# Performance work log

Hardware: AMD Instinct MI355X
Metric: run time of the kernel (lower is better)

The kernel has to match this reference:

```python
import jax, jax.numpy as jnp
import numpy as np

N = 20000
CIN = 32
COUT = 64
K = 4              # kernel_size per axis
KF = K * K * K     # 64 kernel bins
EXTENT = 0.1       # filter_extent; search radius = EXTENT/2
E_PAD = 262144
FOUR_OVER_PI = 4.0 / np.pi
EPS = 1e-12


def _safe_sqrt(x):
    # sqrt with zero (not nan) gradient at 0
    return jnp.sqrt(jnp.maximum(x, EPS))


def ball_to_cube_vp(p):
    """Open3D ball_to_cube_volume_preserving: unit ball -> [-1,1]^3 cube.
    p: [E,3] points in the unit ball."""
    x, y, z = p[:, 0], p[:, 1], p[:, 2]
    sq = x * x + y * y + z * z
    norm = _safe_sqrt(sq)
    rxy2 = x * x + y * y
    # --- sphere -> cylinder (volume preserving) ---
    top = 1.25 * z * z > rxy2
    s_top = _safe_sqrt(3.0 * norm / (norm + jnp.abs(z) + EPS))
    s_side = norm / _safe_sqrt(rxy2)
    cx = jnp.where(top, x * s_top, x * s_side)
    cy = jnp.where(top, y * s_top, y * s_side)
    cz = jnp.where(top, jnp.sign(z) * norm, 1.5 * z)
    zero = sq < EPS
    cx = jnp.where(zero, 0.0, cx)
    cy = jnp.where(zero, 0.0, cy)
    cz = jnp.where(zero, 0.0, cz)
    # --- cylinder -> cube (angle preserving square mapping in xy) ---
    rxy = _safe_sqrt(cx * cx + cy * cy)
    xbig = jnp.abs(cy) <= jnp.abs(cx)
    safe_x = jnp.where(jnp.abs(cx) > EPS, cx, 1.0)
    safe_y = jnp.where(jnp.abs(cy) > EPS, cy, 1.0)
    qx = jnp.sign(cx) * rxy
    qy = jnp.sign(cy) * rxy
    bx = jnp.where(xbig, qx, qy * FOUR_OVER_PI * jnp.arctan(cx / safe_y))
    by = jnp.where(xbig, qx * FOUR_OVER_PI * jnp.arctan(cy / safe_x), qy)
    small = cx * cx + cy * cy < EPS
    bx = jnp.where(small, 0.0, bx)
    by = jnp.where(small, 0.0, by)
    return jnp.stack([bx, by, cz], axis=1)


def setup_inputs() -> dict:
    rng = np.random.default_rng(0)
    pos = rng.random((N, 3)).astype(np.float32)
    radius = EXTENT * 0.5
    # chunked brute-force fixed-radius search (ignore self pairs)
    sq_norms = (pos * pos).sum(-1)
    qs, ns = [], []
    chunk = 2000
    for s in range(0, N, chunk):
        blk = pos[s:s + chunk]
        d2 = sq_norms[s:s + chunk, None] + sq_norms[None, :] - 2.0 * blk @ pos.T
        qi, nj = np.nonzero(d2 < radius * radius)
        qi = qi + s
        keep = qi != nj
        qs.append(qi[keep]); ns.append(nj[keep])
    eq = np.concatenate(qs); en = np.concatenate(ns)
    E = eq.shape[0]
    assert E <= E_PAD, E
    edge_q = np.zeros(E_PAD, np.int64); edge_q[:E] = eq
    edge_n = np.zeros(E_PAD, np.int64); edge_n[:E] = en
    edge_valid = np.zeros(E_PAD, np.float32); edge_valid[:E] = 1.0

    key = jax.random.key(0)
    k1, k2, k3, k4 = jax.random.split(key, 4)
    feats = jax.random.normal(k1, (N, CIN), dtype=jnp.float32)
    Wconv = jax.random.normal(k2, (K, K, K, CIN, COUT), dtype=jnp.float32) * 0.05
    Wd = jax.random.normal(k3, (CIN, COUT), dtype=jnp.float32) * 0.05
    bd = jax.random.normal(k4, (COUT,), dtype=jnp.float32) * 0.05
    return {"feats": feats, "pos": jnp.asarray(pos), "Wconv": Wconv,
            "Wd": Wd, "bd": bd,
            "edge_q": jnp.asarray(edge_q), "edge_n": jnp.asarray(edge_n),
            "edge_valid": jnp.asarray(edge_valid)}


def _cconv(feats, pos, Wconv, edge_q, edge_n, edge_valid):
    # relative positions scaled into the unit ball (search radius = EXTENT/2)
    rel = (pos[edge_n] - pos[edge_q]) * (2.0 / EXTENT)          # [E,3]
    cube = ball_to_cube_vp(rel)                                  # [E,3] in [-1,1]^3
    # align_corners=True grid coords
    u = jnp.clip((cube + 1.0) * 0.5 * (K - 1), 0.0, K - 1.0)     # [E,3] (x,y,z)
    i0 = jnp.clip(jnp.floor(u).astype(jnp.int32), 0, K - 2)
    f = u - i0.astype(u.dtype)                                   # trilinear fracs
    fj = feats[edge_n] * edge_valid[:, None]                     # [E,Cin]
    segq = edge_q.astype(jnp.int32) * KF
    # accumulate neighbor feats into per-query kernel bins (8 trilinear corners)
    Z = jnp.zeros((N * KF, CIN), feats.dtype)
    for dz in (0, 1):
        wz = f[:, 2] if dz else 1.0 - f[:, 2]
        for dy in (0, 1):
            wy = f[:, 1] if dy else 1.0 - f[:, 1]
            for dx in (0, 1):
                wx = f[:, 0] if dx else 1.0 - f[:, 0]
                w = wz * wy * wx
                idx = ((i0[:, 2] + dz) * K + (i0[:, 1] + dy)) * K + (i0[:, 0] + dx)
                Z = Z + jax.ops.segment_sum(fj * w[:, None], segq + idx,
                                            num_segments=N * KF)
    # dense contraction against the flattened filter bank
    return jnp.einsum('nki,kio->no', Z.reshape(N, KF, CIN),
                      Wconv.reshape(KF, CIN, COUT))


def reference(feats, pos, Wconv, Wd, bd, edge_q, edge_n, edge_valid):
    ans_conv = _cconv(feats, pos, Wconv, edge_q, edge_n, edge_valid)
    ans_dense = feats @ Wd + bd
    return ans_conv, ans_dense
```

## Files before the change

kernel.cpp:

```cpp
#include <hip/hip_runtime.h>

#define N_PTS 20000
#define CIN   32
#define COUT  64
#define KK    4
#define KF    64
#define KDIM  2048
#define E_PAD 262144
#define EPS   1e-12f
#define FOUR_OVER_PI 1.27323954473516f
#define QB    8
#define MT16  16

#define NB_Q 1024
#define NB_G 1024
#define NB_W 512
#define NB_F 1250
#define NB_D 313

typedef __attribute__((ext_vector_type(8))) short bf16x8;
typedef __attribute__((ext_vector_type(4))) float f32x4;

__device__ __forceinline__ float sgnf(float v) {
    return v > 0.f ? 1.f : (v < 0.f ? -1.f : 0.f);
}
__device__ __forceinline__ int imin(int a, int b) { return a < b ? a : b; }
__device__ __forceinline__ int imax(int a, int b) { return a > b ? a : b; }

__device__ __forceinline__ unsigned short f2bf(float f) {
    unsigned u = __float_as_uint(f);
    u = u + 0x7fffu + ((u >> 16) & 1u);
    return (unsigned short)(u >> 16);
}

__device__ __forceinline__ unsigned cvtpk(float a, float b) {
    unsigned r;
    asm("v_cvt_pk_bf16_f32 %0, %1, %2" : "=v"(r) : "v"(a), "v"(b));
    return r;
}

__device__ __forceinline__ void edge_geom(
    const float* __restrict__ pos, int n, int q,
    int& cellb, float& ofx, float& ofy, float& ofz)
{
    const float rx = (pos[n * 3 + 0] - pos[q * 3 + 0]) * 20.f;
    const float ry = (pos[n * 3 + 1] - pos[q * 3 + 1]) * 20.f;
    const float rz = (pos[n * 3 + 2] - pos[q * 3 + 2]) * 20.f;
    const float sq   = rx * rx + ry * ry + rz * rz;
    const float nrm  = sqrtf(fmaxf(sq, EPS));
    const float rxy2 = rx * rx + ry * ry;
    const bool  top  = (1.25f * rz * rz > rxy2);
    const float s_top  = sqrtf(fmaxf(3.f * nrm / (nrm + fabsf(rz) + EPS), EPS));
    const float s_side = nrm / sqrtf(fmaxf(rxy2, EPS));
    float cx = top ? rx * s_top : rx * s_side;
    float cy = top ? ry * s_top : ry * s_side;
    float cz = top ? sgnf(rz) * nrm : 1.5f * rz;
    if (sq < EPS) { cx = 0.f; cy = 0.f; cz = 0.f; }
    const float rc2 = cx * cx + cy * cy;
    const float rxy = sqrtf(fmaxf(rc2, EPS));
    const bool  xbig = fabsf(cy) <= fabsf(cx);
    const float safe_x = (fabsf(cx) > EPS) ? cx : 1.f;
    const float safe_y = (fabsf(cy) > EPS) ? cy : 1.f;
    const float qxv = sgnf(cx) * rxy;
    const float qyv = sgnf(cy) * rxy;
    float bx = xbig ? qxv : qyv * FOUR_OVER_PI * atanf(cx / safe_y);
    float by = xbig ? qxv * FOUR_OVER_PI * atanf(cy / safe_x) : qyv;
    if (rc2 < EPS) { bx = 0.f; by = 0.f; }
    const float ux = fminf(fmaxf((bx + 1.f) * 0.5f * 3.f, 0.f), 3.f);
    const float uy = fminf(fmaxf((by + 1.f) * 0.5f * 3.f, 0.f), 3.f);
    const float uz = fminf(fmaxf((cz + 1.f) * 0.5f * 3.f, 0.f), 3.f);
    const int ix = imin(imax((int)floorf(ux), 0), 2);
    const int iy = imin(imax((int)floorf(uy), 0), 2);
    const int iz = imin(imax((int)floorf(uz), 0), 2);
    cellb = (iz * KK + iy) * KK + ix;
    ofx = ux - (float)ix; ofy = uy - (float)iy; ofz = uz - (float)iz;
}

__global__ __launch_bounds__(256) void prologue_kernel(
    const float* __restrict__ feats, const float* __restrict__ pos,
    const float* __restrict__ Wconv, const float* __restrict__ Wd,
    const float* __restrict__ bd,
    const int* __restrict__ eq, const int* __restrict__ en,
    const float* __restrict__ ev, int strideQ, int strideN,
    int* __restrict__ qstart, unsigned short* __restrict__ Wfrag,
    unsigned* __restrict__ fbp, float4* __restrict__ rec,
    float* __restrict__ out)
{
    const int bid = blockIdx.x;
    const int tid = threadIdx.x;
    if (bid < NB_Q) {
        const int e = bid * 256 + tid;
        int k = (ev[e] > 0.f) ? eq[e * strideQ] : N_PTS;
        if (k > N_PTS) k = N_PTS;
        int kp = -1;
        if (e > 0) {
            kp = (ev[e - 1] > 0.f) ? eq[(e - 1) * strideQ] : N_PTS;
            if (kp > N_PTS) kp = N_PTS;
        }
        for (int q = kp + 1; q <= k; ++q) qstart[q] = e;
        if (e == E_PAD - 1)
            for (int q = k + 1; q <= N_PTS; ++q) qstart[q] = E_PAD;
    } else if (bid < NB_Q + NB_G) {
        const int e = (bid - NB_Q) * 256 + tid;
        const int q = eq[e * strideQ];
        const int n = en[e * strideN];
        int ib; float fx, fy, fz;
        edge_geom(pos, n, q, ib, fx, fy, fz);
        float4 r;
        r.x = fx; r.y = fy; r.z = fz;
        r.w = __int_as_float(n | (ib << 16) | (1 << 22));
        rec[e] = r;
    } else if (bid < NB_Q + NB_G + NB_W) {
        const int idx = (bid - NB_Q - NB_G) * 256 + tid;
        const int j    = idx & 7;
        const int lane = (idx >> 3) & 63;
        const int nf   = (idx >> 9) & 3;
        const int ks   = idx >> 11;
        const int k    = ks * 32 + ((lane >> 4) << 3) + j;
        const int col  = nf * 16 + (lane & 15);
        Wfrag[idx] = f2bf(Wconv[k * COUT + col]);
    } else if (bid < NB_Q + NB_G + NB_W + NB_F) {
        const int i = (bid - NB_Q - NB_G - NB_W) * 256 + tid;
        const int n = i >> 4, c = i & 15;
        fbp[i] = cvtpk(feats[n * CIN + c], feats[n * CIN + c + 16]);
    } else {
        const int db   = bid - NB_Q - NB_G - NB_W - NB_F;
        const int wv   = tid >> 6, lane = tid & 63;
        const int r16  = lane & 15, kgrp = lane >> 4;
        const int qb   = (db * 4 + wv) * 16;
        if (qb < N_PTS) {
            const float4 f0 = *(const float4*)(feats + (size_t)(qb + r16) * CIN + kgrp * 8);
            const float4 f1 = *(const float4*)(feats + (size_t)(qb + r16) * CIN + kgrp * 8 + 4);
            bf16x8 a8;
            ((unsigned*)&a8)[0] = cvtpk(f0.x, f0.y);
            ((unsigned*)&a8)[1] = cvtpk(f0.z, f0.w);
            ((unsigned*)&a8)[2] = cvtpk(f1.x, f1.y);
            ((unsigned*)&a8)[3] = cvtpk(f1.z, f1.w);
            #pragma unroll
            for (int nf = 0; nf < 4; ++nf) {
                bf16x8 b8;
                #pragma unroll
                for (int jp = 0; jp < 4; ++jp) {
                    const float w0 = Wd[(kgrp * 8 + jp * 2)     * COUT + nf * 16 + r16];
                    const float w1 = Wd[(kgrp * 8 + jp * 2 + 1) * COUT + nf * 16 + r16];
                    ((unsigned*)&b8)[jp] = cvtpk(w0, w1);
                }
                f32x4 acc = {0.f, 0.f, 0.f, 0.f};
                acc = __builtin_amdgcn_mfma_f32_16x16x32_bf16(a8, b8, acc, 0, 0, 0);
                const float bo = bd[nf * 16 + r16];
                #pragma unroll
                for (int rg = 0; rg < 4; ++rg) {
                    const int q = qb + kgrp * 4 + rg;
                    out[(size_t)N_PTS * COUT + q * COUT + nf * 16 + r16] = acc[rg] + bo;
                }
            }
        }
    }
}

__global__ __launch_bounds__(512, 4) void fused_kernel(
    const unsigned* __restrict__ fbp,
    const float4* __restrict__ rec,
    const unsigned short* __restrict__ Wfrag,
    const int* __restrict__ qstart, float* __restrict__ out)
{
    __shared__ __align__(16) unsigned short Zl[MT16 * KDIM];
    __shared__ __align__(16) char scratch[8192];
    float4 (*ebuf)[2][32]   = (float4 (*)[2][32])scratch;
    float  (*partial)[MT16][COUT] = (float (*)[MT16][COUT])scratch;

    const int t    = threadIdx.x;
    const int w    = t >> 6;
    const int lane = t & 63;
    const int r16  = lane & 15;
    const int kgrp = lane >> 4;
    const int q0   = blockIdx.x * MT16;

    const int dxc = r16 & 3, dyc = r16 >> 2;
    {
        const int lo0 = qstart[q0 + w * 2];
        const int hi0 = qstart[q0 + w * 2 + 1];
        const int hi1 = qstart[q0 + w * 2 + 2];
        const int lo1 = hi0;
        const int nch0 = imax(1, (hi0 - lo0 + 31) >> 5);
        const int nch1 = imax(1, (hi1 - lo1 + 31) >> 5);
        const int NC   = nch0 + nch1;

        {
            const int sfi = lane >> 5, l32 = lane & 31;
            const int isq1 = sfi >= nch0;
            const int c    = isq1 ? sfi - nch0 : sfi;
            const int lo   = isq1 ? lo1 : lo0;
            const int hi   = isq1 ? hi1 : hi0;
            const int e    = lo + c * 32 + l32;
            float4 r;
            if (e < hi) r = rec[e];
            else { r.x = 0.f; r.y = 0.f; r.z = 0.f; r.w = __int_as_float(0); }
            ebuf[w][sfi][l32] = r;
        }

        f32x4 acc[2][4];
        #pragma unroll
        for (int mf = 0; mf < 2; ++mf)
            #pragma unroll
            for (int nf = 0; nf < 4; ++nf)
                acc[mf][nf] = (f32x4){0.f, 0.f, 0.f, 0.f};

        for (int fi = 0; fi < NC; ++fi) {
            if (fi == nch0) {
                const int qs = w * 2;
                #pragma unroll
                for (int mf = 0; mf < 2; ++mf)
                    #pragma unroll
                    for (int nf = 0; nf < 4; ++nf) {
                        uint2 dv;
                        dv.x = cvtpk(acc[mf][nf][0], acc[mf][nf][1]);
                        dv.y = cvtpk(acc[mf][nf][2], acc[mf][nf][3]);
                        const int g      = nf * 16 + r16;
                        const int slot   = g * 64 + qs * 4 + mf * 2 + (kgrp >> 1);
                        const int stored = slot ^ (g & 7);
                        *(uint2*)&Zl[stored * 8 + (kgrp & 1) * 4] = dv;
                        acc[mf][nf] = (f32x4){0.f, 0.f, 0.f, 0.f};
                    }
            }
            const float4* buf = ebuf[w][fi & 1];
            bf16x8 bP[4], af[2];
            #pragma unroll
            for (int jp = 0; jp < 4; ++jp) {
                float p[2][4];
                #pragma unroll
                for (int h = 0; h < 2; ++h) {
                    const int j = jp * 2 + h;
                    const float4 r = buf[kgrp * 8 + j];
                    const int meta = __float_as_int(r.w);
                    const int n    = meta & 0xFFFF;
                    const int ib   = (meta >> 16) & 63;
                    const float valid = (meta & (1 << 22)) ? 1.f : 0.f;
                    const int ix = ib & 3, iy = (ib >> 2) & 3, iz = ib >> 4;
                    const float wx = (dxc == ix) ? (1.f - r.x)
                                   : ((dxc == ix + 1) ? r.x : 0.f);
                    const float wy = (dyc == iy) ? (1.f - r.y)
                                   : ((dyc == iy + 1) ? r.y : 0.f);
                    const float wxy = wx * wy * valid;
                    const float z0 = wxy * (1.f - r.z), z1 = wxy * r.z;
                    p[h][0] = (iz == 0) ? z0 : 0.f;
                    p[h][1] = (iz == 0) ? z1 : ((iz == 1) ? z0 : 0.f);
                    p[h][2] = (iz == 2) ? z0 : ((iz == 1) ? z1 : 0.f);
                    p[h][3] = (iz == 2) ? z1 : 0.f;
                    const unsigned uf = fbp[(size_t)n * 16 + r16];
                    af[0][j] = (short)(uf & 0xFFFFu);
                    af[1][j] = (short)(uf >> 16);
                }
                #pragma unroll
                for (int nf = 0; nf < 4; ++nf)
                    ((unsigned*)&bP[nf])[jp] = cvtpk(p[0][nf], p[1][nf]);
            }
            #pragma unroll
            for (int nf = 0; nf < 4; ++nf) {
                acc[0][nf] = __builtin_amdgcn_mfma_f32_16x16x32_bf16(
                    af[0], bP[nf], acc[0][nf], 0, 0, 0);
                acc[1][nf] = __builtin_amdgcn_mfma_f32_16x16x32_bf16(
                    af[1], bP[nf], acc[1][nf], 0, 0, 0);
            }
            const int nfi = fi + 2;
            if (nfi < NC && lane < 32) {
                const int isq1 = nfi >= nch0;
                const int c    = isq1 ? nfi - nch0 : nfi;
                const int lo   = isq1 ? lo1 : lo0;
                const int hi   = isq1 ? hi1 : hi0;
                const int e    = lo + c * 32 + lane;
                float4 r;
                if (e < hi) r = rec[e];
                else { r.x = 0.f; r.y = 0.f; r.z = 0.f;
                       r.w = __int_as_float(0); }
                ebuf[w][fi & 1][lane] = r;
            }
        }
        {
            const int qs = w * 2 + 1;
            #pragma unroll
            for (int mf = 0; mf < 2; ++mf)
                #pragma unroll
                for (int nf = 0; nf < 4; ++nf) {
                    uint2 dv;
                    dv.x = cvtpk(acc[mf][nf][0], acc[mf][nf][1]);
                    dv.y = cvtpk(acc[mf][nf][2], acc[mf][nf][3]);
                    const int g      = nf * 16 + r16;
                    const int slot   = g * 64 + qs * 4 + mf * 2 + (kgrp >> 1);
                    const int stored = slot ^ (g & 7);
                    *(uint2*)&Zl[stored * 8 + (kgrp & 1) * 4] = dv;
                }
        }
    }
    __syncthreads();

    {
        const int kw  = w >> 2;
        const int nfB = w & 3;
        f32x4 acc0 = {0.f, 0.f, 0.f, 0.f};
        f32x4 acc1 = {0.f, 0.f, 0.f, 0.f};
        #pragma unroll 4
        for (int i = 0; i < 16; ++i) {
            const int ksA = kw * 32 + 2 * i;
            const int ksB = ksA + 1;
            const int stA = (ksA * 64 + r16 * 4 + kgrp) ^ (ksA & 7);
            const int stB = (ksB * 64 + r16 * 4 + kgrp) ^ (ksB & 7);
            const bf16x8 aA = *(const bf16x8*)&Zl[stA * 8];
            const bf16x8 aB = *(const bf16x8*)&Zl[stB * 8];
            const bf16x8 bA =
                *(const bf16x8*)(Wfrag + (((ksA * 4 + nfB) * 64) + lane) * 8);
            const bf16x8 bB =
                *(const bf16x8*)(Wfrag + (((ksB * 4 + nfB) * 64) + lane) * 8);
            acc0 = __builtin_amdgcn_mfma_f32_16x16x32_bf16(aA, bA, acc0, 0, 0, 0);
            acc1 = __builtin_amdgcn_mfma_f32_16x16x32_bf16(aB, bB, acc1, 0, 0, 0);
        }
        const f32x4 accB = acc0 + acc1;
        #pragma unroll
        for (int rg = 0; rg < 4; ++rg)
            partial[kw][kgrp * 4 + rg][nfB * 16 + r16] = accB[rg];
    }
    __syncthreads();

    #pragma unroll
    for (int rep = 0; rep < MT16 * COUT / 512; ++rep) {
        const int idx = rep * 512 + t;
        const int r = idx >> 6, o = idx & 63;
        out[(q0 + r) * COUT + o] = partial[0][r][o] + partial[1][r][o];
    }
}

__global__ __launch_bounds__(256) void conv_dense_kernel(
    const float* __restrict__ feats, const float* __restrict__ pos,
    const float* __restrict__ Wconv, const float* __restrict__ Wd,
    const float* __restrict__ bd,
    const int* __restrict__ en, const float* __restrict__ ev,
    const int* __restrict__ qstart, int strideN,
    float* __restrict__ out)
{
    __shared__ float Z[QB][KF][CIN];
    __shared__ float partial[4][QB][COUT];
    __shared__ int   rec_n[256], rec_b[256];
    __shared__ float rec_fx[256], rec_fy[256], rec_fz[256];
    __shared__ int   qs9[QB + 1];

    const int t = threadIdx.x, wave = t >> 6, lane = t & 63;
    const int q0 = blockIdx.x * QB;
    if (t <= QB) qs9[t] = qstart[q0 + t];
    float* zf = &Z[0][0][0];
    for (int j = t; j < QB * KF * CIN; j += 256) zf[j] = 0.f;
    __syncthreads();
    const int eLo = qs9[0], eHi = qs9[QB];
    const int ci = lane & 31, dbase = lane >> 5;
    for (int cb = eLo; cb < eHi; cb += 256) {
        const int cnt = imin(256, eHi - cb);
        if (t < cnt) {
            const int e = cb + t;
            int q = q0;
            #pragma unroll
            for (int s = 1; s < QB; ++s) if (e >= qs9[s]) q = q0 + s;
            int nn = ((const int*)en)[e];
            int ib; float fx, fy, fz;
            edge_geom(pos, nn, q, ib, fx, fy, fz);
            rec_n[t] = nn; rec_b[t] = ib;
            rec_fx[t] = fx; rec_fy[t] = fy; rec_fz[t] = fz;
        }
        __syncthreads();
        for (int s = 0; s < QB / 4; ++s) {
            const int qs = wave * (QB / 4) + s;
            const int lo = imax(qs9[qs], cb);
            const int hi = imin(qs9[qs + 1], cb + cnt);
            for (int e = lo; e < hi; ++e) {
                const int r = e - cb;
                const int n = rec_n[r], ib = rec_b[r];
                const float fx = rec_fx[r], fy = rec_fy[r], fz = rec_fz[r];
                const float fj = feats[n * CIN + ci];
                const float wxf = dbase ? fx : 1.f - fx;
                #pragma unroll
                for (int dd = 0; dd < 4; ++dd) {
                    const int dy = dd & 1, dz = dd >> 1;
                    const float wv = (dz ? fz : 1.f - fz) * (dy ? fy : 1.f - fy) * wxf;
                    Z[qs][ib + dz * 16 + dy * 4 + dbase][ci] += fj * wv;
                }
            }
        }
        __syncthreads();
    }
    float acc[QB];
    #pragma unroll
    for (int qs = 0; qs < QB; ++qs) acc[qs] = 0.f;
    const int o = lane;
    for (int kk = 0; kk < KF / 4; ++kk) {
        const int kf = wave * (KF / 4) + kk;
        #pragma unroll
        for (int ii = 0; ii < CIN; ii += 4) {
            float4 z4[QB];
            #pragma unroll
            for (int qs = 0; qs < QB; ++qs)
                z4[qs] = *(const float4*)&Z[qs][kf][ii];
            #pragma unroll
            for (int c = 0; c < 4; ++c) {
                const float wv = Wconv[(kf * CIN + ii + c) * COUT + o];
                #pragma unroll
                for (int qs = 0; qs < QB; ++qs)
                    acc[qs] += wv * ((const float*)&z4[qs])[c];
            }
        }
    }
    #pragma unroll
    for (int qs = 0; qs < QB; ++qs) partial[wave][qs][o] = acc[qs];
    __syncthreads();
    for (int s = 0; s < QB / 4; ++s) {
        const int qs = wave * (QB / 4) + s;
        const int q  = q0 + qs;
        out[q * COUT + o] = partial[0][qs][o] + partial[1][qs][o] +
                            partial[2][qs][o] + partial[3][qs][o];
        float dacc = bd[o];
        #pragma unroll
        for (int ii = 0; ii < CIN; ++ii)
            dacc += feats[q * CIN + ii] * Wd[ii * COUT + o];
        out[N_PTS * COUT + q * COUT + o] = dacc;
    }
}

__global__ __launch_bounds__(256) void pack_en_kernel(
    const int* __restrict__ en, int stride, int* __restrict__ en32)
{
    const int e = blockIdx.x * 256 + threadIdx.x;
    if (e < E_PAD) en32[e] = en[e * stride];
}

__global__ __launch_bounds__(256) void build_qstart_kernel(
    const int* __restrict__ eq, const float* __restrict__ ev,
    int stride, int* __restrict__ qstart)
{
    int e = blockIdx.x * 256 + threadIdx.x;
    if (e >= E_PAD) return;
    int k = (ev[e] > 0.f) ? eq[e * stride] : N_PTS;
    if (k > N_PTS) k = N_PTS;
    int kp = -1;
    if (e > 0) {
        kp = (ev[e - 1] > 0.f) ? eq[(e - 1) * stride] : N_PTS;
        if (kp > N_PTS) kp = N_PTS;
    }
    for (int q = kp + 1; q <= k; ++q) qstart[q] = e;
    if (e == E_PAD - 1) {
        for (int q = k + 1; q <= N_PTS; ++q) qstart[q] = E_PAD;
    }
}

extern "C" void kernel_launch(void* const* d_in, const int* in_sizes, int n_in,
                              void* d_out, int out_size, void* d_ws, size_t ws_size,
                              hipStream_t stream)
{
    const float* feats = (const float*)d_in[0];
    const float* pos   = (const float*)d_in[1];
    const float* Wconv = (const float*)d_in[2];
    const float* Wd    = (const float*)d_in[3];
    const float* bd    = (const float*)d_in[4];
    const int*   eq    = (const int*)d_in[5];
    const int*   en    = (const int*)d_in[6];
    const float* ev    = (const float*)d_in[7];
    const int strideQ = in_sizes[5] / E_PAD;
    const int strideN = in_sizes[6] / E_PAD;

    int* qstart = (int*)d_ws;
    const size_t offW  = 81920;
    const size_t offFB = offW + 262144;
    const size_t offR  = offFB + (size_t)N_PTS * CIN * 2;
    const size_t needed = offR + (size_t)E_PAD * 16;

    if (ws_size >= needed) {
        unsigned short* Wfrag = (unsigned short*)((char*)d_ws + offW);
        unsigned*       fbp   = (unsigned*)((char*)d_ws + offFB);
        float4*         rec   = (float4*)((char*)d_ws + offR);
        prologue_kernel<<<NB_Q + NB_G + NB_W + NB_F + NB_D, 256, 0, stream>>>(
            feats, pos, Wconv, Wd, bd, eq, en, ev, strideQ, strideN,
            qstart, Wfrag, fbp, rec, (float*)d_out);
        fused_kernel<<<N_PTS / MT16, 512, 0, stream>>>(
            fbp, rec, Wfrag, qstart, (float*)d_out);
    } else {
        build_qstart_kernel<<<E_PAD / 256, 256, 0, stream>>>(
            eq, ev, strideQ, qstart);
        int* en32 = (int*)((char*)d_ws + offW);
        pack_en_kernel<<<E_PAD / 256, 256, 0, stream>>>(en, strideN, en32);
        conv_dense_kernel<<<N_PTS / QB, 256, 0, stream>>>(
            feats, pos, Wconv, Wd, bd, en32, ev, qstart, 1, (float*)d_out);
    }
}
```

Measured before the change: 36.82 us.

## Shrink fused tile to 8 queries, one query per wave, drop edge prefetch

The fused conv kernel now handles 8 queries per 512-thread block instead of 16, so each wave owns a single query rather than two. This removes the mid-loop accumulator flush and the double-buffered edge-record prefetch. The grid doubles, giving more blocks and finer load balance across varying neighbor counts. In exchange, the dense GEMM stage computes 16-row MFMA tiles with only 8 valid rows, wasting half its work, and edge loads are no longer overlapped with compute. The prologue also skips geometry for invalid edges, which leaves their record slots unwritten.

```diff
diff --git a/kernel.cpp b/kernel.cpp
--- a/kernel.cpp
+++ b/kernel.cpp
@@ -10,7 +10,7 @@
 #define EPS   1e-12f
 #define FOUR_OVER_PI 1.27323954473516f
 #define QB    8
-#define MT16  16
+#define MT8   8
 
 #define NB_Q 1024
 #define NB_G 1024
@@ -102,14 +102,16 @@
             for (int q = k + 1; q <= N_PTS; ++q) qstart[q] = E_PAD;
     } else if (bid < NB_Q + NB_G) {
         const int e = (bid - NB_Q) * 256 + tid;
-        const int q = eq[e * strideQ];
-        const int n = en[e * strideN];
-        int ib; float fx, fy, fz;
-        edge_geom(pos, n, q, ib, fx, fy, fz);
-        float4 r;
-        r.x = fx; r.y = fy; r.z = fz;
-        r.w = __int_as_float(n | (ib << 16) | (1 << 22));
-        rec[e] = r;
+        if (ev[e] > 0.f) {
+            const int q = eq[e * strideQ];
+            const int n = en[e * strideN];
+            int ib; float fx, fy, fz;
+            edge_geom(pos, n, q, ib, fx, fy, fz);
+            float4 r;
+            r.x = fx; r.y = fy; r.z = fz;
+            r.w = __int_as_float(n | (ib << 16) | (1 << 22));
+            rec[e] = r;
+        }
     } else if (bid < NB_Q + NB_G + NB_W) {
         const int idx = (bid - NB_Q - NB_G) * 256 + tid;
         const int j    = idx & 7;
@@ -164,40 +166,23 @@
     const unsigned short* __restrict__ Wfrag,
     const int* __restrict__ qstart, float* __restrict__ out)
 {
-    __shared__ __align__(16) unsigned short Zl[MT16 * KDIM];
-    __shared__ __align__(16) char scratch[8192];
-    float4 (*ebuf)[2][32]   = (float4 (*)[2][32])scratch;
-    float  (*partial)[MT16][COUT] = (float (*)[MT16][COUT])scratch;
+    __shared__ __align__(16) unsigned short Zl[MT8 * KDIM];
+    __shared__ __align__(16) char scratch[4096];
+    float4 (*ebuf)[32]           = (float4 (*)[32])scratch;
+    float  (*partial)[MT8][COUT] = (float (*)[MT8][COUT])scratch;
 
     const int t    = threadIdx.x;
     const int w    = t >> 6;
     const int lane = t & 63;
     const int r16  = lane & 15;
     const int kgrp = lane >> 4;
-    const int q0   = blockIdx.x * MT16;
+    const int q0   = blockIdx.x * MT8;
 
     const int dxc = r16 & 3, dyc = r16 >> 2;
     {
-        const int lo0 = qstart[q0 + w * 2];
-        const int hi0 = qstart[q0 + w * 2 + 1];
-        const int hi1 = qstart[q0 + w * 2 + 2];
-        const int lo1 = hi0;
-        const int nch0 = imax(1, (hi0 - lo0 + 31) >> 5);
-        const int nch1 = imax(1, (hi1 - lo1 + 31) >> 5);
-        const int NC   = nch0 + nch1;
-
-        {
-            const int sfi = lane >> 5, l32 = lane & 31;
-            const int isq1 = sfi >= nch0;
-            const int c    = isq1 ? sfi - nch0 : sfi;
-            const int lo   = isq1 ? lo1 : lo0;
-            const int hi   = isq1 ? hi1 : hi0;
-            const int e    = lo + c * 32 + l32;
-            float4 r;
-            if (e < hi) r = rec[e];
-            else { r.x = 0.f; r.y = 0.f; r.z = 0.f; r.w = __int_as_float(0); }
-            ebuf[w][sfi][l32] = r;
-        }
+        const int lo  = qstart[q0 + w];
+        const int hi  = qstart[q0 + w + 1];
+        const int nch = imax(1, (hi - lo + 31) >> 5);
 
         f32x4 acc[2][4];
         #pragma unroll
@@ -206,24 +191,15 @@
             for (int nf = 0; nf < 4; ++nf)
                 acc[mf][nf] = (f32x4){0.f, 0.f, 0.f, 0.f};
 
-        for (int fi = 0; fi < NC; ++fi) {
-            if (fi == nch0) {
-                const int qs = w * 2;
-                #pragma unroll
-                for (int mf = 0; mf < 2; ++mf)
-                    #pragma unroll
-                    for (int nf = 0; nf < 4; ++nf) {
-                        uint2 dv;
-                        dv.x = cvtpk(acc[mf][nf][0], acc[mf][nf][1]);
-                        dv.y = cvtpk(acc[mf][nf][2], acc[mf][nf][3]);
-                        const int g      = nf * 16 + r16;
-                        const int slot   = g * 64 + qs * 4 + mf * 2 + (kgrp >> 1);
-                        const int stored = slot ^ (g & 7);
-                        *(uint2*)&Zl[stored * 8 + (kgrp & 1) * 4] = dv;
-                        acc[mf][nf] = (f32x4){0.f, 0.f, 0.f, 0.f};
-                    }
-            }
-            const float4* buf = ebuf[w][fi & 1];
+        for (int c = 0; c < nch; ++c) {
+            if (lane < 32) {
+                const int e = lo + c * 32 + lane;
+                float4 r;
+                if (e < hi) r = rec[e];
+                else { r.x = 0.f; r.y = 0.f; r.z = 0.f;
+                       r.w = __int_as_float(0); }
+                ebuf[w][lane] = r;
+            }
             bf16x8 bP[4], af[2];
             #pragma unroll
             for (int jp = 0; jp < 4; ++jp) {
@@ -231,7 +207,7 @@
                 #pragma unroll
                 for (int h = 0; h < 2; ++h) {
                     const int j = jp * 2 + h;
-                    const float4 r = buf[kgrp * 8 + j];
+                    const float4 r = ebuf[w][kgrp * 8 + j];
                     const int meta = __float_as_int(r.w);
                     const int n    = meta & 0xFFFF;
                     const int ib   = (meta >> 16) & 63;
@@ -262,49 +238,34 @@
                 acc[1][nf] = __builtin_amdgcn_mfma_f32_16x16x32_bf16(
                     af[1], bP[nf], acc[1][nf], 0, 0, 0);
             }
-            const int nfi = fi + 2;
-            if (nfi < NC && lane < 32) {
-                const int isq1 = nfi >= nch0;
-                const int c    = isq1 ? nfi - nch0 : nfi;
-                const int lo   = isq1 ? lo1 : lo0;
-                const int hi   = isq1 ? hi1 : hi0;
-                const int e    = lo + c * 32 + lane;
-                float4 r;
-                if (e < hi) r = rec[e];
-                else { r.x = 0.f; r.y = 0.f; r.z = 0.f;
-                       r.w = __int_as_float(0); }
-                ebuf[w][fi & 1][lane] = r;
-            }
-        }
-        {
-            const int qs = w * 2 + 1;
-            #pragma unroll
-            for (int mf = 0; mf < 2; ++mf)
-                #pragma unroll
-                for (int nf = 0; nf < 4; ++nf) {
-                    uint2 dv;
-                    dv.x = cvtpk(acc[mf][nf][0], acc[mf][nf][1]);
-                    dv.y = cvtpk(acc[mf][nf][2], acc[mf][nf][3]);
-                    const int g      = nf * 16 + r16;
-                    const int slot   = g * 64 + qs * 4 + mf * 2 + (kgrp >> 1);
-                    const int stored = slot ^ (g & 7);
-                    *(uint2*)&Zl[stored * 8 + (kgrp & 1) * 4] = dv;
-                }
-        }
+        }
+        #pragma unroll
+        for (int mf = 0; mf < 2; ++mf)
+            #pragma unroll
+            for (int nf = 0; nf < 4; ++nf) {
+                uint2 dv;
+                dv.x = cvtpk(acc[mf][nf][0], acc[mf][nf][1]);
+                dv.y = cvtpk(acc[mf][nf][2], acc[mf][nf][3]);
+                const int g      = nf * 16 + r16;
+                const int slot   = g * 32 + w * 4 + mf * 2 + (kgrp >> 1);
+                const int stored = slot ^ (g & 7);
+                *(uint2*)&Zl[stored * 8 + (kgrp & 1) * 4] = dv;
+            }
     }
     __syncthreads();
 
     {
         const int kw  = w >> 2;
         const int nfB = w & 3;
+        const int rr  = r16 & 7;
         f32x4 acc0 = {0.f, 0.f, 0.f, 0.f};
         f32x4 acc1 = {0.f, 0.f, 0.f, 0.f};
         #pragma unroll 4
         for (int i = 0; i < 16; ++i) {
             const int ksA = kw * 32 + 2 * i;
             const int ksB = ksA + 1;
-            const int stA = (ksA * 64 + r16 * 4 + kgrp) ^ (ksA & 7);
-            const int stB = (ksB * 64 + r16 * 4 + kgrp) ^ (ksB & 7);
+            const int stA = (ksA * 32 + rr * 4 + kgrp) ^ (ksA & 7);
+            const int stB = (ksB * 32 + rr * 4 + kgrp) ^ (ksB & 7);
             const bf16x8 aA = *(const bf16x8*)&Zl[stA * 8];
             const bf16x8 aB = *(const bf16x8*)&Zl[stB * 8];
             const bf16x8 bA =
@@ -316,15 +277,16 @@
         }
         const f32x4 accB = acc0 + acc1;
         #pragma unroll
-        for (int rg = 0; rg < 4; ++rg)
-            partial[kw][kgrp * 4 + rg][nfB * 16 + r16] = accB[rg];
+        for (int rg = 0; rg < 4; ++rg) {
+            const int row = kgrp * 4 + rg;
+            if (row < MT8)
+                partial[kw][row][nfB * 16 + r16] = accB[rg];
+        }
     }
     __syncthreads();
 
-    #pragma unroll
-    for (int rep = 0; rep < MT16 * COUT / 512; ++rep) {
-        const int idx = rep * 512 + t;
-        const int r = idx >> 6, o = idx & 63;
+    {
+        const int r = t >> 6, o = t & 63;
         out[(q0 + r) * COUT + o] = partial[0][r][o] + partial[1][r][o];
     }
 }
@@ -476,7 +438,7 @@
         prologue_kernel<<<NB_Q + NB_G + NB_W + NB_F + NB_D, 256, 0, stream>>>(
             feats, pos, Wconv, Wd, bd, eq, en, ev, strideQ, strideN,
             qstart, Wfrag, fbp, rec, (float*)d_out);
-        fused_kernel<<<N_PTS / MT16, 512, 0, stream>>>(
+        fused_kernel<<<N_PTS / MT8, 512, 0, stream>>>(
             fbp, rec, Wfrag, qstart, (float*)d_out);
     } else {
         build_qstart_kernel<<<E_PAD / 256, 256, 0, stream>>>(
```

Result: slower. 42.57 us (+15.6%).
